# Kernel tuning notes

Hardware: AMD Instinct MI355X
Metric: run time of the kernel (lower is better)

Reference implementation:

```python
import jax, jax.numpy as jnp
import numpy as np
from math import factorial as _f, sqrt as _msqrt

N = 2000000
JA, JB, JC, JD = 1, 1, 0, 1
PA, PB, PC, PD = -1, -1, -1, -1
M0_B, M0_C, M0_D = 2.01026, 0.13957061, 2.00685
# (name, chain, m0, g0, J, Par) -- static resonance table (init_kwargs res)
RES = [("Zc_4025", -1, 4.026, 0.025, 1, 1),
       ("D2_2460", 21, 2.4607, 0.0475, 2, 1),
       ("D1_2420", 121, 2.4232, 0.025, 1, 1)]

def cg_coef(j1, j2, m1, m2, j, m):
    if m1 + m2 != m or j < abs(j1 - j2) or j > j1 + j2:
        return 0.0
    if abs(m1) > j1 or abs(m2) > j2 or abs(m) > j:
        return 0.0
    pref = _msqrt((2 * j + 1) * _f(j1 + j2 - j) * _f(j + j1 - j2) * _f(j + j2 - j1) / _f(j1 + j2 + j + 1))
    pref *= _msqrt(_f(j + m) * _f(j - m) * _f(j1 - m1) * _f(j1 + m1) * _f(j2 - m2) * _f(j2 + m2))
    s = 0.0
    for k in range(max(0, j2 - j - m1, j1 + m2 - j), min(j1 + j2 - j, j1 - m1, j2 + m2) + 1):
        s += (-1) ** k / (_f(k) * _f(j1 + j2 - j - k) * _f(j1 - m1 - k) * _f(j2 + m2 - k) * _f(j - j2 + m1 + k) * _f(j - j1 - m2 + k))
    return pref * s

def wigner_d(j, m1, m2, c):
    # d^j_{m1,m2}(theta) with cos(theta)=c, theta in [0, pi]
    ch = jnp.sqrt((1.0 + c) * 0.5)
    sh = jnp.sqrt((1.0 - c) * 0.5)
    pref = _msqrt(_f(j + m1) * _f(j - m1) * _f(j + m2) * _f(j - m2))
    out = None
    for s in range(max(0, m2 - m1), min(j - m1, j + m2) + 1):
        coef = pref * (-1) ** (m1 - m2 + s) / (_f(j + m2 - s) * _f(s) * _f(m1 - m2 + s) * _f(j - m1 - s))
        t = coef * ch ** (2 * j + m2 - m1 - 2 * s) * sh ** (m1 - m2 + 2 * s)
        out = t if out is None else out + t
    return out

def ls_list(ja, jb, jc, pa, pb, pc):
    dl = 0 if pa * pb * pc == 1 else 1
    out = []
    for s in range(abs(jb - jc), jb + jc + 1):
        for l in range(abs(ja - s), ja + s + 1):
            if l % 2 == dl:
                out.append((l, s))
    return out

def _build_layout():
    layout, off = [], 0
    for (_, chain, m0, g0, J, Par) in RES:
        jc, jd, je = (0, 1, 1) if chain < 0 else ((1, 1, 0) if chain < 100 else (1, 0, 1))
        ls0 = ls_list(JA, J, jc, PA, Par, -1)
        ls1 = ls_list(J, jd, je, Par, -1, -1)
        layout.append(((off, ls0), (off + len(ls0), ls1)))
        off += len(ls0) + len(ls1)
    return layout, off

LAYOUT, NCOEF = _build_layout()

def H_ls(params, entry, ja, jb, jc, lb, lc):
    off, ls = entry
    tot, nz = 0.0, False
    for idx, (l, s) in enumerate(ls):
        c = cg_coef(jb, jc, lb, -lc, s, lb - lc) * cg_coef(l, s, 0, lb - lc, ja, lb - lc)
        if c != 0.0:
            nz = True
            tot = tot + c * jax.lax.complex(params[off + idx, 0], params[off + idx, 1])
    return tot, nz

def getp(M0, M1, M2):
    s, d = M1 + M2, M1 - M2
    p = (M0 - s) * (M0 + s) * (M0 - d) * (M0 + d)
    return jnp.sqrt((p + jnp.abs(p)) * 0.5) / (2.0 * M0)

def bw(m, m0, g0, q, q0):
    gamma = g0 * (q / q0) * (m0 / m)  # L=0 -> Bprime == 1
    num = jax.lax.complex(m0 * gamma, jnp.zeros_like(gamma))
    den = jax.lax.complex((m0 + m) * (m0 - m), -m0 * gamma)
    return num / den

def amp2(m_BC, m_BD, m_CD, cosTheta_BC, cosTheta_B_BC, phi_BC, phi_B_BC, cosTheta_BD, cosTheta_D_BD, phi_D_BD, cosTheta_CD, cosTheta_C_CD, phi_CD, phi_C_CD, cosTheta1, cosTheta2, phi1, phi2, params):
    bws = []
    for (_, chain, m0, g0, J, Par) in RES:
        if chain < 0:
            bws.append(bw(m_BD, m0, g0, getp(m_BD, M0_B, M0_D), getp(m0, M0_B, M0_D)))
        elif chain < 100:
            bws.append(bw(m_BC, m0, g0, getp(m_BC, M0_B, M0_C), getp(m0, M0_B, M0_C)))
        else:
            bws.append(bw(m_CD, m0, g0, getp(m_CD, M0_C, M0_D), getp(m0, M0_C, M0_D)))
    angles = {"BD": cosTheta_BD, "D_BD": cosTheta_D_BD, "BC": cosTheta_BC, "B_BC": cosTheta_B_BC,
              "CD": cosTheta_CD, "C_CD": cosTheta_C_CD, "t1": cosTheta1, "t2": cosTheta2}
    phis = {"D_BD": phi_D_BD, "BC": phi_BC, "B_BC": phi_B_BC, "CD": phi_CD, "C_CD": phi_C_CD, "p1": phi1, "p2": phi2}
    dcache, pcache = {}, {}
    def dfun(j, m1, m2, ang):
        if abs(m1) > j or abs(m2) > j:
            return None
        key = (j, m1, m2, ang)
        if key not in dcache:
            dcache[key] = wigner_d(j, m1, m2, angles[ang])
        return dcache[key]
    def cexp(lam, name):
        if lam == 0:
            return 1.0
        key = (lam, name)
        if key not in pcache:
            ph = -float(lam) * phis[name]
            pcache[key] = jax.lax.complex(jnp.cos(ph), jnp.sin(ph))
        return pcache[key]
    total = 0.0
    for lA in range(-JA, JA + 1, 2):
        for lB in range(-JB, JB + 1):
            for lC in range(-JC, JC + 1):
                for lD in range(-JD, JD + 1):
                    amp = jnp.zeros_like(m_BC, dtype=jnp.complex64)
                    for ri, (_, chain, m0, g0, J, Par) in enumerate(RES):
                        e0, e1 = LAYOUT[ri]
                        ar = None
                        if chain < 0:
                            for lDB in range(-J, J + 1):
                                H1, f1 = H_ls(params, e0, JA, J, JC, lDB, lC)
                                H2, f2 = H_ls(params, e1, J, JD, JB, lD, lB)
                                d1 = dfun(JA, lA, lDB - lC, "BD")
                                d2 = dfun(J, lDB, lD - lB, "D_BD")
                                if not (f1 and f2) or d1 is None or d2 is None:
                                    continue
                                t = (H1 * H2) * (cexp(lD, "D_BD") * (d1 * d2))
                                ar = t if ar is None else ar + t
                        elif chain < 100:
                            for lBC in range(-J, J + 1):
                                for lB2 in range(-JB, JB + 1):
                                    H1, f1 = H_ls(params, e0, JA, J, JD, lBC, lD)
                                    H2, f2 = H_ls(params, e1, J, JB, JC, lB2, lC)
                                    da = dfun(JB, lB2, lB, "t1")
                                    d1 = dfun(JA, lA, lBC - lD, "BC")
                                    d2 = dfun(J, lBC, lB2 - lC, "B_BC")
                                    if not (f1 and f2) or da is None or d1 is None or d2 is None:
                                        continue
                                    t = (H1 * H2) * (cexp(lB2, "p1") * cexp(lBC, "BC") * cexp(lB2, "B_BC") * (da * d1 * d2))
                                    ar = t if ar is None else ar + t
                        else:
                            for lCD in range(-J, J + 1):
                                for lC2 in range(-JD, JD + 1):
                                    H1, f1 = H_ls(params, e0, JA, J, JB, lCD, lB)
                                    H2, f2 = H_ls(params, e1, J, JC, JD, lC, lC2)
                                    da = dfun(JD, lC2, lD, "t2")
                                    d1 = dfun(JA, lA, lCD - lB, "CD")
                                    d2 = dfun(J, lCD, lC2 - lC, "C_CD")
                                    if not (f1 and f2) or da is None or d1 is None or d2 is None:
                                        continue
                                    t = (H1 * H2) * (cexp(lC2, "p2") * cexp(lCD, "CD") * cexp(lC2, "C_CD") * (da * d1 * d2))
                                    ar = t if ar is None else ar + t
                        if ar is not None:
                            amp = amp + ar * bws[ri]
                    total = total + jnp.real(amp) ** 2 + jnp.imag(amp) ** 2
    return total

def setup_inputs():
    key = jax.random.key(0)
    ks = jax.random.split(key, 19)
    u = lambda k, lo, hi: jax.random.uniform(k, (N,), jnp.float32, lo, hi)
    PI = float(np.pi)
    return {
        "m_BC": u(ks[0], 2.17, 2.70),
        "m_BD": u(ks[1], 4.03, 4.25),
        "m_CD": u(ks[2], 2.17, 2.70),
        "cosTheta_BC": u(ks[3], -1.0, 1.0),
        "cosTheta_B_BC": u(ks[4], -1.0, 1.0),
        "phi_BC": u(ks[5], -PI, PI),
        "phi_B_BC": u(ks[6], -PI, PI),
        "cosTheta_BD": u(ks[7], -1.0, 1.0),
        "cosTheta_D_BD": u(ks[8], -1.0, 1.0),
        "phi_D_BD": u(ks[9], -PI, PI),
        "cosTheta_CD": u(ks[10], -1.0, 1.0),
        "cosTheta_C_CD": u(ks[11], -1.0, 1.0),
        "phi_CD": u(ks[12], -PI, PI),
        "phi_C_CD": u(ks[13], -PI, PI),
        "cosTheta1": u(ks[14], -1.0, 1.0),
        "cosTheta2": u(ks[15], -1.0, 1.0),
        "phi1": u(ks[16], -PI, PI),
        "phi2": u(ks[17], -PI, PI),
        "params": jax.random.normal(ks[18], (NCOEF, 2), jnp.float32) * 0.5,
    }

def reference(m_BC, m_BD, m_CD, cosTheta_BC, cosTheta_B_BC, phi_BC, phi_B_BC, cosTheta_BD, cosTheta_D_BD, phi_D_BD, cosTheta_CD, cosTheta_C_CD, phi_CD, phi_C_CD, cosTheta1, cosTheta2, phi1, phi2, params):
    return amp2(m_BC, m_BD, m_CD, cosTheta_BC, cosTheta_B_BC, phi_BC, phi_B_BC, cosTheta_BD, cosTheta_D_BD, phi_D_BD, cosTheta_CD, cosTheta_C_CD, phi_CD, phi_C_CD, cosTheta1, cosTheta2, phi1, phi2, params)
```

## Files before the change

### kernel.cpp

```cpp
#include <hip/hip_runtime.h>
#include <utility>
#include <type_traits>

typedef float f2 __attribute__((ext_vector_type(2)));

constexpr int cabs_i(int x){ return x < 0 ? -x : x; }
constexpr int cmax_i(int a, int b){ return a > b ? a : b; }
constexpr int cmin_i(int a, int b){ return a < b ? a : b; }
constexpr double cfact(int n){ double r = 1.0; for (int i = 2; i <= n; ++i) r *= (double)i; return r; }
constexpr double csqrt_d(double x){
  if (x <= 0.0) return 0.0;
  double r = x > 1.0 ? x : 1.0;
  for (int i = 0; i < 64; ++i) r = 0.5 * (r + x / r);
  return r;
}
constexpr double cg_coef(int j1,int j2,int m1,int m2,int j,int m){
  if (m1 + m2 != m || j < cabs_i(j1 - j2) || j > j1 + j2) return 0.0;
  if (cabs_i(m1) > j1 || cabs_i(m2) > j2 || cabs_i(m) > j) return 0.0;
  double pref = csqrt_d((2.0*j + 1.0) * cfact(j1+j2-j) * cfact(j+j1-j2) * cfact(j+j2-j1) / cfact(j1+j2+j+1));
  pref *= csqrt_d(cfact(j+m)*cfact(j-m)*cfact(j1-m1)*cfact(j1+m1)*cfact(j2-m2)*cfact(j2+m2));
  double s = 0.0;
  const int k0 = cmax_i(0, cmax_i(j2-j-m1, j1+m2-j));
  const int k1 = cmin_i(j1+j2-j, cmin_i(j1-m1, j2+m2));
  for (int k = k0; k <= k1; ++k){
    double t = 1.0/(cfact(k)*cfact(j1+j2-j-k)*cfact(j1-m1-k)*cfact(j2+m2-k)*cfact(j-j2+m1+k)*cfact(j-j1-m2+k));
    s += (k & 1) ? -t : t;
  }
  return pref * s;
}
constexpr double wd_coef(int j,int m1,int m2,int s){
  double pref = csqrt_d(cfact(j+m1)*cfact(j-m1)*cfact(j+m2)*cfact(j-m2));
  double c = pref / (cfact(j+m2-s)*cfact(s)*cfact(m1-m2+s)*cfact(j-m1-s));
  return ((m1-m2+s) & 1) ? -c : c;
}
constexpr double cgetp(double M0,double M1,double M2){
  double s = M1+M2, d = M1-M2;
  double p = (M0-s)*(M0+s)*(M0-d)*(M0+d);
  double pp = 0.5*(p + (p < 0 ? -p : p));
  return csqrt_d(pp)/(2.0*M0);
}

template<int Start, class F, int... Is>
__device__ inline void static_for_impl(F&& f, std::integer_sequence<int, Is...>){
  (f(std::integral_constant<int, Start + Is>{}), ...);
}
template<int Start, int End, class F>
__device__ inline void static_for(F&& f){
  if constexpr (End > Start)
    static_for_impl<Start>(static_cast<F&&>(f), std::make_integer_sequence<int, End - Start>{});
}

__device__ inline f2 vfma2(f2 a, f2 b, f2 c){ return __builtin_elementwise_fma(a, b, c); }

struct cplx { f2 v; };
__device__ inline cplx operator+(cplx a, cplx b){ return { a.v + b.v }; }
__device__ inline cplx operator*(cplx a, cplx b){
  f2 sw  = { -a.v.y, a.v.x };
  f2 bre = {  b.v.x, b.v.x };
  f2 bim = {  b.v.y, b.v.y };
  return { vfma2(a.v, bre, sw * bim) };
}
__device__ inline cplx cconj(cplx a){ return { f2{ a.v.x, -a.v.y } }; }
__device__ inline cplx cscale(cplx x, float r){ return { x.v * f2{r, r} }; }
__device__ inline void caxpy(cplx& acc, float r, cplx x){
  acc.v = vfma2(f2{r, r}, x.v, acc.v);
}

template<int n> __device__ inline float spow(float x){
  if constexpr (n <= 0) return 1.f;
  else return x * spow<n-1>(x);
}
template<int n> __device__ inline f2 vpow(f2 x){
  if constexpr (n <= 0) return f2{1.f, 1.f};
  else return x * vpow<n-1>(x);
}

struct angs { float u, v, hp; };
__device__ inline angs mkang1(float c){
  angs A;
  A.u = (1.f + c) * 0.5f;
  A.v = (1.f - c) * 0.5f;
  A.hp = __builtin_amdgcn_sqrtf(A.u * A.v);
  return A;
}
struct angp { f2 u, v, hp; };
__device__ inline angp mkang2(f2 c){
  angp A;
  A.u = (c + 1.f) * 0.5f;
  A.v = (1.f - c) * 0.5f;
  f2 p = A.u * A.v;
  A.hp = f2{ __builtin_amdgcn_sqrtf(p.x), __builtin_amdgcn_sqrtf(p.y) };
  return A;
}
template<int j, int m1, int m2>
__device__ inline float wigs(const angs& A){
  constexpr int s0 = cmax_i(0, m2 - m1);
  constexpr int s1 = cmin_i(j - m1, j + m2);
  float out = 0.f;
  static_for<s0, s1 + 1>([&](auto S){
    constexpr int s = decltype(S)::value;
    constexpr float coef = (float)wd_coef(j, m1, m2, s);
    constexpr int P = 2*j + m2 - m1 - 2*s;
    constexpr int Q = m1 - m2 + 2*s;
    float mono;
    if constexpr (P & 1) mono = A.hp * spow<(P-1)/2>(A.u) * spow<(Q-1)/2>(A.v);
    else                 mono = spow<P/2>(A.u) * spow<Q/2>(A.v);
    out = fmaf(coef, mono, out);
  });
  return out;
}
template<int j, int m1, int m2>
__device__ inline f2 wig(const angp& A){
  constexpr int s0 = cmax_i(0, m2 - m1);
  constexpr int s1 = cmin_i(j - m1, j + m2);
  f2 out = {0.f, 0.f};
  static_for<s0, s1 + 1>([&](auto S){
    constexpr int s = decltype(S)::value;
    constexpr float coef = (float)wd_coef(j, m1, m2, s);
    constexpr int P = 2*j + m2 - m1 - 2*s;
    constexpr int Q = m1 - m2 + 2*s;
    f2 mono;
    if constexpr (P & 1) mono = A.hp * vpow<(P-1)/2>(A.u) * vpow<(Q-1)/2>(A.v);
    else                 mono = vpow<P/2>(A.u) * vpow<Q/2>(A.v);
    out = vfma2(f2{coef, coef}, mono, out);
  });
  return out;
}

struct LS { int l, s; };
template<int E> struct Entry;
template<> struct Entry<0>{ static constexpr int off = 0;  static constexpr int n = 2; static constexpr LS ls[2] = {{0,1},{2,1}}; };
template<> struct Entry<1>{ static constexpr int off = 2;  static constexpr int n = 3; static constexpr LS ls[3] = {{0,1},{2,1},{2,2}}; };
template<> struct Entry<2>{ static constexpr int off = 5;  static constexpr int n = 5; static constexpr LS ls[5] = {{0,1},{2,1},{2,2},{2,3},{4,3}}; };
template<> struct Entry<3>{ static constexpr int off = 10; static constexpr int n = 1; static constexpr LS ls[1] = {{2,1}}; };
template<> struct Entry<4>{ static constexpr int off = 11; static constexpr int n = 3; static constexpr LS ls[3] = {{0,1},{2,1},{2,2}}; };
template<> struct Entry<5>{ static constexpr int off = 14; static constexpr int n = 2; static constexpr LS ls[2] = {{0,1},{2,1}}; };

template<int E,int ja,int jb,int jc,int lb,int lc>
constexpr double hcoef(int idx){
  return cg_coef(jb, jc, lb, -lc, Entry<E>::ls[idx].s, lb - lc)
       * cg_coef(Entry<E>::ls[idx].l, Entry<E>::ls[idx].s, 0, lb - lc, ja, lb - lc);
}
template<int E,int ja,int jb,int jc,int lb,int lc>
constexpr bool hnz(){
  bool any = false;
  for (int i = 0; i < Entry<E>::n; ++i) if (hcoef<E,ja,jb,jc,lb,lc>(i) != 0.0) any = true;
  return any;
}
template<int E,int ja,int jb,int jc,int lb,int lc>
__device__ inline cplx H_ls(const cplx* par){
  cplx tot{ f2{0.f, 0.f} };
  static_for<0, Entry<E>::n>([&](auto I){
    constexpr double c = hcoef<E,ja,jb,jc,lb,lc>(decltype(I)::value);
    if constexpr (c != 0.0){
      caxpy(tot, (float)c, par[Entry<E>::off + decltype(I)::value]);
    }
  });
  return tot;
}

constexpr int IH10(int lDB){ return lDB+1; }
constexpr int IH20(int lD,int lB){ return 3+(lD+1)*3+(lB+1); }
constexpr int IH11(int lBC,int lD){ return 12+(lBC+2)*3+(lD+1); }
constexpr int IH21(int lB2){ return 27+(lB2+1)/2; }
constexpr int IH12(int lCD,int lB){ return 29+(lCD+1)*3+(lB+1); }
constexpr int IH22(int lC2){ return 38+(lC2+1); }
constexpr int NH = 41;

__device__ inline void compute_htab(const float2* __restrict__ g_par, cplx* t){
  cplx par[16];
  #pragma unroll
  for (int k = 0; k < 16; ++k){ float2 p = g_par[k]; par[k].v = f2{p.x, p.y}; }
  static_for<-1,2>([&](auto L){ constexpr int l = decltype(L)::value; t[IH10(l)] = H_ls<0,1,1,0,l,0>(par); });
  static_for<-1,2>([&](auto D){ constexpr int lD = decltype(D)::value;
    static_for<-1,2>([&](auto B){ constexpr int lB = decltype(B)::value;
      t[IH20(lD,lB)] = H_ls<1,1,1,1,lD,lB>(par); }); });
  static_for<-2,3>([&](auto C){ constexpr int lBC = decltype(C)::value;
    static_for<-1,2>([&](auto D){ constexpr int lD = decltype(D)::value;
      t[IH11(lBC,lD)] = H_ls<2,1,2,1,lBC,lD>(par); }); });
  t[IH21(-1)] = H_ls<3,2,1,0,-1,0>(par);
  t[IH21( 1)] = H_ls<3,2,1,0, 1,0>(par);
  static_for<-1,2>([&](auto C){ constexpr int lCD = decltype(C)::value;
    static_for<-1,2>([&](auto B){ constexpr int lB = decltype(B)::value;
      t[IH12(lCD,lB)] = H_ls<4,1,1,1,lCD,lB>(par); }); });
  static_for<-1,2>([&](auto C){ constexpr int lC2 = decltype(C)::value;
    t[IH22(lC2)] = H_ls<5,1,0,1,0,lC2>(par); });
}

template<int IDX, bool PRE>
__device__ inline cplx getH(const float2* __restrict__ hs, const cplx* ht){
  if constexpr (PRE){ float2 v = hs[IDX]; return cplx{ f2{v.x, v.y} }; }
  else return ht[IDX];
}
#define GH(IDX) getH<(IDX), PRE>(hs, ht)

constexpr double dM0B = 2.01026, dM0C = 0.13957061, dM0D = 2.00685;
constexpr double dR0m0 = 4.026,  dR0g0 = 0.025;
constexpr double dR1m0 = 2.4607, dR1g0 = 0.0475;
constexpr double dR2m0 = 2.4232, dR2g0 = 0.025;

constexpr float M0SQ0 = (float)(dR0m0*dR0m0);
constexpr float M0SQ1 = (float)(dR1m0*dR1m0);
constexpr float M0SQ2 = (float)(dR2m0*dR2m0);
constexpr float S2_0 = (float)((dM0B+dM0D)*(dM0B+dM0D)), D2_0 = (float)((dM0B-dM0D)*(dM0B-dM0D));
constexpr float S2_1 = (float)((dM0B+dM0C)*(dM0B+dM0C)), D2_1 = (float)((dM0B-dM0C)*(dM0B-dM0C));
constexpr float S2_2 = (float)((dM0C+dM0D)*(dM0C+dM0D)), D2_2 = (float)((dM0C-dM0D)*(dM0C-dM0D));
constexpr float K0 = (float)(2.0 * cgetp(dR0m0, dM0B, dM0D) / (dR0g0 * dR0m0 * dR0m0));
constexpr float K1 = (float)(2.0 * cgetp(dR1m0, dM0B, dM0C) / (dR1g0 * dR1m0 * dR1m0));
constexpr float K2 = (float)(2.0 * cgetp(dR2m0, dM0C, dM0D) / (dR2g0 * dR2m0 * dR2m0));

__device__ inline void bw_eval2(f2 m, f2 K, f2 m0sq, f2 S2, f2 D2, cplx& o0, cplx& o1){
  f2 m2 = m * m;
  f2 t  = m0sq - m2;
  f2 p  = (m2 - S2) * (m2 - D2);
  f2 pp = f2{ fmaxf(p.x, 0.f), fmaxf(p.y, 0.f) };
  f2 rs = f2{ __builtin_amdgcn_rsqf(pp.x), __builtin_amdgcn_rsqf(pp.y) };
  f2 r  = K * t * m2 * rs;
  float i0 = __builtin_amdgcn_rcpf(fmaf(r.x, r.x, 1.f));
  float i1 = __builtin_amdgcn_rcpf(fmaf(r.y, r.y, 1.f));
  o0 = { f2{ r.x * i0, i0 } };
  o1 = { f2{ r.y * i1, i1 } };
}
__device__ inline cplx bw_eval(float m, float K, float m0sq, float S2, float D2){
  float m2 = m * m;
  float t  = m0sq - m2;
  float p  = (m2 - S2) * (m2 - D2);
  float pp = fmaxf(p, 0.f);
  float r  = K * t * m2 * __builtin_amdgcn_rsqf(pp);
  float inv = __builtin_amdgcn_rcpf(fmaf(r, r, 1.f));
  return { f2{ r * inv, inv } };
}
__device__ inline cplx phase_neg(float phi){
  return { f2{ __cosf(phi), -__sinf(phi) } };
}

__global__ void prep_htab_kernel(const float2* __restrict__ g_par, float2* __restrict__ ws){
  if (blockIdx.x != 0 || threadIdx.x != 0) return;
  cplx t[NH];
  compute_htab(g_par, t);
  #pragma unroll
  for (int k = 0; k < NH; ++k) ws[k] = make_float2(t[k].v.x, t[k].v.y);
}

template<bool PRE>
__global__ void __launch_bounds__(256, 4)
AllAmplitude_59665685676511_kernel(
    const float* __restrict__ g_mBC,  const float* __restrict__ g_mBD,  const float* __restrict__ g_mCD,
    const float* __restrict__ g_cBC,  const float* __restrict__ g_cBBC, const float* __restrict__ g_pBC,  const float* __restrict__ g_pBBC,
    const float* __restrict__ g_cBD,  const float* __restrict__ g_cDBD, const float* __restrict__ g_pDBD,
    const float* __restrict__ g_cCD,  const float* __restrict__ g_cCCD, const float* __restrict__ g_pCD,  const float* __restrict__ g_pCCD,
    const float* __restrict__ g_cT1,  const float* __restrict__ g_cT2,  const float* __restrict__ g_p1,   const float* __restrict__ g_p2,
    const float2* __restrict__ g_par, const float2* __restrict__ hs,
    float* __restrict__ out, int n)
{
  int i = blockIdx.x * 256 + threadIdx.x;
  if (i >= n) return;

  cplx ht[NH];
  if constexpr (!PRE) compute_htab(g_par, ht);

  angp PBDT1  = mkang2(f2{ g_cBD[i], g_cT1[i]  });
  angp PT2CCD = mkang2(f2{ g_cT2[i], g_cCCD[i] });
  angp PBCCD  = mkang2(f2{ g_cBC[i], g_cCD[i]  });
  angs SDBD   = mkang1(g_cDBD[i]);
  angs SBBC   = mkang1(g_cBBC[i]);

  f2 dBDT1[2][3];
  static_for<0,2>([&](auto R_){ constexpr int r = decltype(R_)::value; constexpr int m1 = 2*r-1;
    static_for<-1,2>([&](auto M_){ constexpr int m2 = decltype(M_)::value;
      dBDT1[r][m2+1] = wig<1, m1, m2>(PBDT1); }); });
  f2 dT2CCD[3][3];
  static_for<-1,2>([&](auto M1_){ constexpr int m1 = decltype(M1_)::value;
    static_for<-1,2>([&](auto M2_){ constexpr int m2 = decltype(M2_)::value;
      dT2CCD[m1+1][m2+1] = wig<1, m1, m2>(PT2CCD); }); });
  f2 dBCCD[2][3];
  static_for<0,2>([&](auto A_){ constexpr int a = decltype(A_)::value; constexpr int lA = 2*a-1;
    static_for<-1,2>([&](auto M_){ constexpr int dm = decltype(M_)::value;
      dBCCD[a][dm+1] = wig<1, lA, dm>(PBCCD); }); });
  float dDBD[3][3], dBBC[5][2];
  static_for<-1,2>([&](auto M1_){ constexpr int m1 = decltype(M1_)::value;
    static_for<-1,2>([&](auto M2_){ constexpr int m2 = decltype(M2_)::value;
      dDBD[m1+1][m2+1] = wigs<1, m1, m2>(SDBD); }); });
  static_for<-2,3>([&](auto C_){ constexpr int lBC = decltype(C_)::value;
    static_for<0,2>([&](auto K_){ constexpr int k = decltype(K_)::value; constexpr int lB2 = 2*k-1;
      dBBC[lBC+2][k] = wigs<2, lBC, lB2>(SBBC); }); });

  cplx G0[2][3];
  {
    cplx P0[3][3];
    static_for<-1,2>([&](auto L_){ constexpr int lDB = decltype(L_)::value;
      cplx h = GH(IH10(lDB));
      static_for<0,3>([&](auto M_){ constexpr int mi = decltype(M_)::value;
        P0[lDB+1][mi] = cscale(h, dDBD[lDB+1][mi]); }); });
    static_for<0,2>([&](auto A_){ constexpr int a = decltype(A_)::value;
      static_for<0,3>([&](auto M_){ constexpr int mi = decltype(M_)::value;
        cplx acc{ f2{0.f, 0.f} };
        static_for<-1,2>([&](auto L_){ constexpr int lDB = decltype(L_)::value;
          caxpy(acc, dBDT1[a][lDB+1].x, P0[lDB+1][mi]);
        });
        G0[a][mi] = acc; }); });
  }

  cplx V1[3][5];
  {
    cplx eP1 = phase_neg(g_p1[i] + g_pBBC[i]);
    cplx U1m = GH(IH21(-1)) * cconj(eP1);
    cplx U1p = GH(IH21( 1)) * eP1;
    cplx Qm[5], Qp[5];
    static_for<-2,3>([&](auto C_){ constexpr int lBC = decltype(C_)::value;
      Qm[lBC+2] = cscale(U1m, dBBC[lBC+2][0]);
      Qp[lBC+2] = cscale(U1p, dBBC[lBC+2][1]); });
    static_for<-1,2>([&](auto B_){ constexpr int lB = decltype(B_)::value;
      static_for<-2,3>([&](auto C_){ constexpr int lBC = decltype(C_)::value;
        cplx acc{ f2{0.f, 0.f} };
        caxpy(acc, dBDT1[0][lB+1].y, Qm[lBC+2]);
        caxpy(acc, dBDT1[1][lB+1].y, Qp[lBC+2]);
        V1[lB+1][lBC+2] = acc; }); });
  }

  cplx V2[3][3];
  {
    cplx eP2 = phase_neg(g_p2[i] + g_pCCD[i]);
    cplx U2[3];
    U2[0] = GH(IH22(-1)) * cconj(eP2);
    U2[1] = GH(IH22(0));
    U2[2] = GH(IH22(1)) * eP2;
    cplx R2t[3][3];
    static_for<-1,2>([&](auto C_){ constexpr int lCD = decltype(C_)::value;
      static_for<-1,2>([&](auto X_){ constexpr int lC2 = decltype(X_)::value;
        R2t[lCD+1][lC2+1] = cscale(U2[lC2+1], dT2CCD[lCD+1][lC2+1].y); }); });
    static_for<-1,2>([&](auto D_){ constexpr int lD = decltype(D_)::value;
      static_for<-1,2>([&](auto C_){ constexpr int lCD = decltype(C_)::value;
        cplx acc{ f2{0.f, 0.f} };
        static_for<-1,2>([&](auto X_){ constexpr int lC2 = decltype(X_)::value;
          caxpy(acc, dT2CCD[lC2+1][lD+1].x, R2t[lCD+1][lC2+1]);
        });
        V2[lD+1][lCD+1] = acc; }); });
  }

  cplx bw0, bw1;
  bw_eval2(f2{ g_mBD[i], g_mBC[i] }, f2{K0, K1}, f2{M0SQ0, M0SQ1},
           f2{S2_0, S2_1}, f2{D2_0, D2_1}, bw0, bw1);
  const cplx bw2 = bw_eval(g_mCD[i], K2, M0SQ2, S2_2, D2_2);

  cplx W0T[3][3] = {};
  {
    const cplx eD = phase_neg(g_pDBD[i]);
    cplx EBW0[3] = { cconj(eD) * bw0, bw0, eD * bw0 };
    static_for<-1,2>([&](auto D_){ constexpr int lD = decltype(D_)::value;
      static_for<-1,2>([&](auto B_){ constexpr int lB = decltype(B_)::value;
        if constexpr (cabs_i(lD - lB) <= 1 && hnz<1,1,1,1,lD,lB>())
          W0T[lD+1][lB+1] = GH(IH20(lD,lB)) * EBW0[lD+1];
      }); });
  }
  cplx HT1[5][3] = {};
  {
    const cplx eBC = phase_neg(g_pBC[i]);
    const cplx e2  = eBC * eBC;
    cplx T1B[5] = { cconj(e2) * bw1, cconj(eBC) * bw1, bw1, eBC * bw1, e2 * bw1 };
    static_for<-2,3>([&](auto C_){ constexpr int lBC = decltype(C_)::value;
      static_for<-1,2>([&](auto D_){ constexpr int lD = decltype(D_)::value;
        if constexpr (cabs_i(lBC - lD) <= 1 && hnz<2,1,2,1,lBC,lD>())
          HT1[lBC+2][lD+1] = GH(IH11(lBC,lD)) * T1B[lBC+2];
      }); });
  }
  cplx HT2[3][3] = {};
  {
    const cplx eCD = phase_neg(g_pCD[i]);
    cplx T2B[3] = { cconj(eCD) * bw2, bw2, eCD * bw2 };
    static_for<-1,2>([&](auto C_){ constexpr int lCD = decltype(C_)::value;
      static_for<-1,2>([&](auto B_){ constexpr int lB = decltype(B_)::value;
        if constexpr (cabs_i(lCD - lB) <= 1 && hnz<4,1,1,1,lCD,lB>())
          HT2[lCD+1][lB+1] = GH(IH12(lCD,lB)) * T2B[lCD+1];
      }); });
  }

  f2 t0 = {0.f, 0.f}, t1 = {0.f, 0.f};
  static_for<-1,2>([&](auto B_){ constexpr int lB = decltype(B_)::value;
    static_for<-1,2>([&](auto D_){ constexpr int lD = decltype(D_)::value;
      cplx Y1[3] = {};
      static_for<-1,2>([&](auto M_){ constexpr int dm = decltype(M_)::value; constexpr int lBC = lD + dm;
        if constexpr (hnz<2,1,2,1,lBC,lD>())
          Y1[dm+1] = HT1[lBC+2][lD+1] * V1[lB+1][lBC+2];
      });
      cplx Y2[3] = {};
      static_for<-1,2>([&](auto M_){ constexpr int dm = decltype(M_)::value; constexpr int lCD = lB + dm;
        if constexpr (cabs_i(lCD) <= 1 && hnz<4,1,1,1,lCD,lB>())
          Y2[dm+1] = HT2[lCD+1][lB+1] * V2[lD+1][lCD+1];
      });
      static_for<0,2>([&](auto A_){ constexpr int a = decltype(A_)::value;
        cplx amp{ f2{0.f, 0.f} };
        if constexpr (cabs_i(lD - lB) <= 1 && hnz<1,1,1,1,lD,lB>())
          amp = W0T[lD+1][lB+1] * G0[a][lD-lB+1];
        static_for<-1,2>([&](auto M_){ constexpr int dm = decltype(M_)::value; constexpr int lBC = lD + dm;
          if constexpr (hnz<2,1,2,1,lBC,lD>())
            caxpy(amp, dBCCD[a][dm+1].x, Y1[dm+1]);
        });
        static_for<-1,2>([&](auto M_){ constexpr int dm = decltype(M_)::value; constexpr int lCD = lB + dm;
          if constexpr (cabs_i(lCD) <= 1 && hnz<4,1,1,1,lCD,lB>())
            caxpy(amp, dBCCD[a][dm+1].y, Y2[dm+1]);
        });
        if constexpr (a == 0) t0 = vfma2(amp.v, amp.v, t0);
        else                  t1 = vfma2(amp.v, amp.v, t1);
      });
    });
  });

  out[i] = (t0.x + t0.y) + (t1.x + t1.y);
}

extern "C" void kernel_launch(void* const* d_in, const int* in_sizes, int n_in,
                              void* d_out, int out_size, void* d_ws, size_t ws_size,
                              hipStream_t stream) {
  (void)n_in; (void)out_size;
  const int n = in_sizes[0];
  const float*  mBC  = (const float*)d_in[0];
  const float*  mBD  = (const float*)d_in[1];
  const float*  mCD  = (const float*)d_in[2];
  const float*  cBC  = (const float*)d_in[3];
  const float*  cBBC = (const float*)d_in[4];
  const float*  pBC  = (const float*)d_in[5];
  const float*  pBBC = (const float*)d_in[6];
  const float*  cBD  = (const float*)d_in[7];
  const float*  cDBD = (const float*)d_in[8];
  const float*  pDBD = (const float*)d_in[9];
  const float*  cCD  = (const float*)d_in[10];
  const float*  cCCD = (const float*)d_in[11];
  const float*  pCD  = (const float*)d_in[12];
  const float*  pCCD = (const float*)d_in[13];
  const float*  cT1  = (const float*)d_in[14];
  const float*  cT2  = (const float*)d_in[15];
  const float*  p1   = (const float*)d_in[16];
  const float*  p2   = (const float*)d_in[17];
  const float2* parm = (const float2*)d_in[18];

  dim3 block(256);
  dim3 grid((n + 255) / 256);

  if (ws_size >= NH * sizeof(float2)) {
    prep_htab_kernel<<<1, 64, 0, stream>>>(parm, (float2*)d_ws);
    AllAmplitude_59665685676511_kernel<true><<<grid, block, 0, stream>>>(
        mBC, mBD, mCD, cBC, cBBC, pBC, pBBC, cBD, cDBD, pDBD,
        cCD, cCCD, pCD, pCCD, cT1, cT2, p1, p2, parm,
        (const float2*)d_ws, (float*)d_out, n);
  } else {
    AllAmplitude_59665685676511_kernel<false><<<grid, block, 0, stream>>>(
        mBC, mBD, mCD, cBC, cBBC, pBC, pBBC, cBD, cDBD, pDBD,
        cCD, cCCD, pCD, pCCD, cT1, cT2, p1, p2, parm,
        nullptr, (float*)d_out, n);
  }
}
```

Baseline: 48.58 us.

## Factor the D2 chain contraction through the rank-2 dBDT1 structure

Restructures the second resonance chain term. The lB dependence enters only through two scalars dBDT1[0/1][lB].y, so the chain can be precontracted into Am/Ap[a][lD] once, outside the lB loop. The inner triple loop then needs only two scalar axpys per amplitude instead of rebuilding V1 and Y1 for every (lB,lD) pair. This cuts complex multiplies, at the cost of reordering the code and changing the float summation order slightly.

```diff
diff --git a/kernel.cpp b/kernel.cpp
--- a/kernel.cpp
+++ b/kernel.cpp
@@ -285,6 +285,53 @@
     static_for<0,2>([&](auto K_){ constexpr int k = decltype(K_)::value; constexpr int lB2 = 2*k-1;
       dBBC[lBC+2][k] = wigs<2, lBC, lB2>(SBBC); }); });
 
+  cplx bw0, bw1;
+  bw_eval2(f2{ g_mBD[i], g_mBC[i] }, f2{K0, K1}, f2{M0SQ0, M0SQ1},
+           f2{S2_0, S2_1}, f2{D2_0, D2_1}, bw0, bw1);
+  const cplx bw2 = bw_eval(g_mCD[i], K2, M0SQ2, S2_2, D2_2);
+
+  cplx Am[2][3], Ap[2][3];
+  {
+    cplx HT1[5][3] = {};
+    {
+      const cplx eBC = phase_neg(g_pBC[i]);
+      const cplx e2  = eBC * eBC;
+      cplx T1B[5] = { cconj(e2) * bw1, cconj(eBC) * bw1, bw1, eBC * bw1, e2 * bw1 };
+      static_for<-2,3>([&](auto C_){ constexpr int lBC = decltype(C_)::value;
+        static_for<-1,2>([&](auto D_){ constexpr int lD = decltype(D_)::value;
+          if constexpr (cabs_i(lBC - lD) <= 1 && hnz<2,1,2,1,lBC,lD>())
+            HT1[lBC+2][lD+1] = GH(IH11(lBC,lD)) * T1B[lBC+2];
+        }); });
+    }
+    cplx eP1 = phase_neg(g_p1[i] + g_pBBC[i]);
+    cplx U1m = GH(IH21(-1)) * cconj(eP1);
+    cplx U1p = GH(IH21( 1)) * eP1;
+    cplx Qm[5], Qp[5];
+    static_for<-2,3>([&](auto C_){ constexpr int lBC = decltype(C_)::value;
+      Qm[lBC+2] = cscale(U1m, dBBC[lBC+2][0]);
+      Qp[lBC+2] = cscale(U1p, dBBC[lBC+2][1]); });
+    cplx Tm[5][3], Tp[5][3];
+    static_for<-2,3>([&](auto C_){ constexpr int lBC = decltype(C_)::value;
+      static_for<-1,2>([&](auto D_){ constexpr int lD = decltype(D_)::value;
+        if constexpr (cabs_i(lBC - lD) <= 1 && hnz<2,1,2,1,lBC,lD>()){
+          Tm[lBC+2][lD+1] = HT1[lBC+2][lD+1] * Qm[lBC+2];
+          Tp[lBC+2][lD+1] = HT1[lBC+2][lD+1] * Qp[lBC+2];
+        }
+      }); });
+    static_for<0,2>([&](auto A_){ constexpr int a = decltype(A_)::value;
+      static_for<-1,2>([&](auto D_){ constexpr int lD = decltype(D_)::value;
+        cplx am{ f2{0.f,0.f} }, ap{ f2{0.f,0.f} };
+        static_for<-1,2>([&](auto M_){ constexpr int dm = decltype(M_)::value; constexpr int lBC = lD + dm;
+          if constexpr (hnz<2,1,2,1,lBC,lD>()){
+            caxpy(am, dBCCD[a][dm+1].x, Tm[lBC+2][lD+1]);
+            caxpy(ap, dBCCD[a][dm+1].x, Tp[lBC+2][lD+1]);
+          }
+        });
+        Am[a][lD+1] = am;
+        Ap[a][lD+1] = ap;
+      }); });
+  }
+
   cplx G0[2][3];
   {
     cplx P0[3][3];
@@ -299,23 +346,6 @@
           caxpy(acc, dBDT1[a][lDB+1].x, P0[lDB+1][mi]);
         });
         G0[a][mi] = acc; }); });
-  }
-
-  cplx V1[3][5];
-  {
-    cplx eP1 = phase_neg(g_p1[i] + g_pBBC[i]);
-    cplx U1m = GH(IH21(-1)) * cconj(eP1);
-    cplx U1p = GH(IH21( 1)) * eP1;
-    cplx Qm[5], Qp[5];
-    static_for<-2,3>([&](auto C_){ constexpr int lBC = decltype(C_)::value;
-      Qm[lBC+2] = cscale(U1m, dBBC[lBC+2][0]);
-      Qp[lBC+2] = cscale(U1p, dBBC[lBC+2][1]); });
-    static_for<-1,2>([&](auto B_){ constexpr int lB = decltype(B_)::value;
-      static_for<-2,3>([&](auto C_){ constexpr int lBC = decltype(C_)::value;
-        cplx acc{ f2{0.f, 0.f} };
-        caxpy(acc, dBDT1[0][lB+1].y, Qm[lBC+2]);
-        caxpy(acc, dBDT1[1][lB+1].y, Qp[lBC+2]);
-        V1[lB+1][lBC+2] = acc; }); });
   }
 
   cplx V2[3][3];
@@ -338,11 +368,6 @@
         V2[lD+1][lCD+1] = acc; }); });
   }
 
-  cplx bw0, bw1;
-  bw_eval2(f2{ g_mBD[i], g_mBC[i] }, f2{K0, K1}, f2{M0SQ0, M0SQ1},
-           f2{S2_0, S2_1}, f2{D2_0, D2_1}, bw0, bw1);
-  const cplx bw2 = bw_eval(g_mCD[i], K2, M0SQ2, S2_2, D2_2);
-
   cplx W0T[3][3] = {};
   {
     const cplx eD = phase_neg(g_pDBD[i]);
@@ -353,17 +378,6 @@
           W0T[lD+1][lB+1] = GH(IH20(lD,lB)) * EBW0[lD+1];
       }); });
   }
-  cplx HT1[5][3] = {};
-  {
-    const cplx eBC = phase_neg(g_pBC[i]);
-    const cplx e2  = eBC * eBC;
-    cplx T1B[5] = { cconj(e2) * bw1, cconj(eBC) * bw1, bw1, eBC * bw1, e2 * bw1 };
-    static_for<-2,3>([&](auto C_){ constexpr int lBC = decltype(C_)::value;
-      static_for<-1,2>([&](auto D_){ constexpr int lD = decltype(D_)::value;
-        if constexpr (cabs_i(lBC - lD) <= 1 && hnz<2,1,2,1,lBC,lD>())
-          HT1[lBC+2][lD+1] = GH(IH11(lBC,lD)) * T1B[lBC+2];
-      }); });
-  }
   cplx HT2[3][3] = {};
   {
     const cplx eCD = phase_neg(g_pCD[i]);
@@ -377,12 +391,9 @@
 
   f2 t0 = {0.f, 0.f}, t1 = {0.f, 0.f};
   static_for<-1,2>([&](auto B_){ constexpr int lB = decltype(B_)::value;
+    const float dT1m = dBDT1[0][lB+1].y;
+    const float dT1p = dBDT1[1][lB+1].y;
     static_for<-1,2>([&](auto D_){ constexpr int lD = decltype(D_)::value;
-      cplx Y1[3] = {};
-      static_for<-1,2>([&](auto M_){ constexpr int dm = decltype(M_)::value; constexpr int lBC = lD + dm;
-        if constexpr (hnz<2,1,2,1,lBC,lD>())
-          Y1[dm+1] = HT1[lBC+2][lD+1] * V1[lB+1][lBC+2];
-      });
       cplx Y2[3] = {};
       static_for<-1,2>([&](auto M_){ constexpr int dm = decltype(M_)::value; constexpr int lCD = lB + dm;
         if constexpr (cabs_i(lCD) <= 1 && hnz<4,1,1,1,lCD,lB>())
@@ -392,10 +403,8 @@
         cplx amp{ f2{0.f, 0.f} };
         if constexpr (cabs_i(lD - lB) <= 1 && hnz<1,1,1,1,lD,lB>())
           amp = W0T[lD+1][lB+1] * G0[a][lD-lB+1];
-        static_for<-1,2>([&](auto M_){ constexpr int dm = decltype(M_)::value; constexpr int lBC = lD + dm;
-          if constexpr (hnz<2,1,2,1,lBC,lD>())
-            caxpy(amp, dBCCD[a][dm+1].x, Y1[dm+1]);
-        });
+        caxpy(amp, dT1m, Am[a][lD+1]);
+        caxpy(amp, dT1p, Ap[a][lD+1]);
         static_for<-1,2>([&](auto M_){ constexpr int dm = decltype(M_)::value; constexpr int lCD = lB + dm;
           if constexpr (cabs_i(lCD) <= 1 && hnz<4,1,1,1,lCD,lB>())
             caxpy(amp, dBCCD[a][dm+1].y, Y2[dm+1]);
```

Result: faster. 47.06 us (-3.1%).
